# Kernel tuning notes

Hardware: AMD Instinct MI355X
Metric: run time of the kernel (lower is better)

Reference implementation:

```python
import jax, jax.numpy as jnp
import numpy as np

D_MODEL = 1024
N_HEADS = 16
HEAD_DIM = D_MODEL // N_HEADS  # 64
THETA = 10000.0
BATCH = 2
SEQ = 2048


def _init_weight(k):
    std = np.sqrt(2.0 / (D_MODEL + D_MODEL)).astype(np.float32)
    return jax.random.truncated_normal(k, -3.0, 3.0, (D_MODEL, D_MODEL), jnp.float32) * std


def setup_inputs() -> dict:
    key = jax.random.key(0)
    kx, kq, kk, kv, ko = jax.random.split(key, 5)
    x = jax.random.normal(kx, (BATCH, SEQ, D_MODEL), jnp.float32)
    token_positions = jnp.arange(SEQ, dtype=jnp.int32)
    return {
        "x": x,
        "token_positions": token_positions,
        "Wq": _init_weight(kq),
        "Wk": _init_weight(kk),
        "Wv": _init_weight(kv),
        "Wo": _init_weight(ko),
    }


def _rope(x, token_positions):
    # x: (B, H, S, HEAD_DIM), token_positions: (S,)
    pair_idx = jnp.arange(0, HEAD_DIM, 2, dtype=jnp.float32)
    inv_freq = 1.0 / (THETA ** (pair_idx / HEAD_DIM))        # (HEAD_DIM/2,)
    angles = token_positions.astype(jnp.float32)[:, None] * inv_freq  # (S, HEAD_DIM/2)
    cos = jnp.cos(angles).astype(x.dtype)
    sin = jnp.sin(angles).astype(x.dtype)
    x_even = x[..., 0::2]
    x_odd = x[..., 1::2]
    out_even = x_even * cos - x_odd * sin
    out_odd = x_even * sin + x_odd * cos
    return jnp.stack((out_even, out_odd), axis=-1).reshape(x.shape)


def reference(x, token_positions, Wq, Wk, Wv, Wo):
    B, S, _ = x.shape

    def proj(W):  # (B,S,D) @ (D,D)^T -> (B,H,S,HEAD_DIM)
        return (x @ W.T).reshape(B, S, N_HEADS, HEAD_DIM).transpose(0, 2, 1, 3)

    q = _rope(proj(Wq), token_positions)
    k = _rope(proj(Wk), token_positions)
    v = proj(Wv)

    scale = 1.0 / np.sqrt(HEAD_DIM).astype(np.float32)
    scores = jnp.einsum('bhqd,bhkd->bhqk', q, k) * scale  # (B,H,S,S)
    causal = jnp.tril(jnp.ones((S, S), dtype=bool))
    scores = jnp.where(causal, scores, -jnp.inf)
    probs = jax.nn.softmax(scores.astype(jnp.float32), axis=-1).astype(x.dtype)

    attn = jnp.einsum('bhqk,bhkd->bhqd', probs, v)  # (B,H,S,HEAD_DIM)
    attn = attn.transpose(0, 2, 1, 3).reshape(B, S, D_MODEL)
    return attn @ Wo.T
```

## Files before the change

### kernel.cpp

```cpp
#include <hip/hip_runtime.h>

typedef __bf16 bf16x4 __attribute__((ext_vector_type(4)));
typedef __bf16 bf16x8 __attribute__((ext_vector_type(8)));
typedef float floatx4 __attribute__((ext_vector_type(4)));

#define MFMA16(a, b, c) __builtin_amdgcn_mfma_f32_16x16x32_bf16((a), (b), (c), 0, 0, 0)

#define GLD16(gptr, lptr)                                                      \
    __builtin_amdgcn_global_load_lds(                                          \
        (const __attribute__((address_space(1))) void*)(gptr),                 \
        (__attribute__((address_space(3))) void*)(lptr), 16, 0, 0)

constexpr int D_MODEL = 1024;
constexpr int SEQ = 2048;
constexpr int HEAD_DIM = 64;
constexpr int M_TOK = 2 * SEQ;
constexpr int N_HEADS = 16;
constexpr float ROPE_C = 0.20762050593048596f;

__global__ __launch_bounds__(256) void convert_all(
    const float* __restrict__ x,  const float* __restrict__ wq,
    const float* __restrict__ wk, const float* __restrict__ wv,
    const float* __restrict__ wo, __bf16* __restrict__ dst,
    const int* __restrict__ pos, float2* __restrict__ rt)
{
    const size_t i = ((size_t)blockIdx.x * 256 + threadIdx.x) * 8;
    const float* s;
    size_t off;
    if (i < 4194304) { s = x; off = i; }
    else {
        const int w = (int)((i - 4194304) >> 20);
        off = (i - 4194304) & 1048575;
        s = (w == 0) ? wq : (w == 1) ? wk : (w == 2) ? wv : wo;
    }
    const floatx4 lo = *(const floatx4*)(s + off);
    const floatx4 hi = *(const floatx4*)(s + off + 4);
    bf16x8 v;
    v[0] = (__bf16)lo[0]; v[1] = (__bf16)lo[1]; v[2] = (__bf16)lo[2]; v[3] = (__bf16)lo[3];
    v[4] = (__bf16)hi[0]; v[5] = (__bf16)hi[1]; v[6] = (__bf16)hi[2]; v[7] = (__bf16)hi[3];
    *(bf16x8*)(dst + i) = v;

    const int gid = blockIdx.x * 256 + threadIdx.x;
    if (gid < SEQ * 32) {
        const int p = gid >> 5, j = gid & 31;
        const float ang = (float)pos[p] * exp2f(-(float)(2 * j) * ROPE_C);
        rt[gid] = make_float2(cosf(ang), sinf(ang));
    }
}

template<int MODE>
__global__ __launch_bounds__(256, 3) void gemm_tiled(
    const __bf16* __restrict__ A, const __bf16* __restrict__ B,
    __bf16* __restrict__ Qb, __bf16* __restrict__ Kb, __bf16* __restrict__ Vt,
    float* __restrict__ Cf, const float2* __restrict__ rt)
{
    __shared__ __bf16 As[128 * 32];
    __shared__ __bf16 Bs[128 * 32];
    const int tid  = threadIdx.x;
    const int wave = tid >> 6, lane = tid & 63;
    const int quad = lane >> 4, l16 = lane & 15;

    constexpr int NWG = (MODE == 0) ? 32 * 24 : 32 * 8;
    const int wgid = blockIdx.x + 32 * blockIdx.y;
    const int nid  = (wgid & 7) * (NWG / 8) + (wgid >> 3);
    const int m0 = (nid & 31) * 128, n0 = (nid >> 5) * 128;
    const int wm = (wave >> 1) * 64, wn = (wave & 1) * 64;

    floatx4 c00 = {}, c01 = {}, c02 = {}, c03 = {};
    floatx4 c10 = {}, c11 = {}, c12 = {}, c13 = {};
    floatx4 c20 = {}, c21 = {}, c22 = {}, c23 = {};
    floatx4 c30 = {}, c31 = {}, c32 = {}, c33 = {};

    const int sm = tid >> 2;
    const int sk = (tid & 3) * 8;
    const __bf16* gA = A + (size_t)(m0 + sm) * D_MODEL + sk;
    const __bf16* gB = B + (size_t)(n0 + sm) * D_MODEL + sk;
    __bf16* lAs0 = &As[wave * 512];
    __bf16* lAs1 = &As[2048 + wave * 512];
    __bf16* lBs0 = &Bs[wave * 512];
    __bf16* lBs1 = &Bs[2048 + wave * 512];

    for (int k0 = 0; k0 < D_MODEL; k0 += 32) {
        __syncthreads();
        GLD16(gA + k0,                          lAs0);
        GLD16(gA + (size_t)64 * D_MODEL + k0,   lAs1);
        GLD16(gB + k0,                          lBs0);
        GLD16(gB + (size_t)64 * D_MODEL + k0,   lBs1);
        __syncthreads();

        const bf16x8 a0 = *(const bf16x8*)&As[(wm      + l16) * 32 + quad * 8];
        const bf16x8 a1 = *(const bf16x8*)&As[(wm + 16 + l16) * 32 + quad * 8];
        const bf16x8 a2 = *(const bf16x8*)&As[(wm + 32 + l16) * 32 + quad * 8];
        const bf16x8 a3 = *(const bf16x8*)&As[(wm + 48 + l16) * 32 + quad * 8];
        const bf16x8 b0 = *(const bf16x8*)&Bs[(wn      + l16) * 32 + quad * 8];
        const bf16x8 b1 = *(const bf16x8*)&Bs[(wn + 16 + l16) * 32 + quad * 8];
        const bf16x8 b2 = *(const bf16x8*)&Bs[(wn + 32 + l16) * 32 + quad * 8];
        const bf16x8 b3 = *(const bf16x8*)&Bs[(wn + 48 + l16) * 32 + quad * 8];

        c00 = MFMA16(a0, b0, c00); c01 = MFMA16(a0, b1, c01);
        c02 = MFMA16(a0, b2, c02); c03 = MFMA16(a0, b3, c03);
        c10 = MFMA16(a1, b0, c10); c11 = MFMA16(a1, b1, c11);
        c12 = MFMA16(a1, b2, c12); c13 = MFMA16(a1, b3, c13);
        c20 = MFMA16(a2, b0, c20); c21 = MFMA16(a2, b1, c21);
        c22 = MFMA16(a2, b2, c22); c23 = MFMA16(a2, b3, c23);
        c30 = MFMA16(a3, b0, c30); c31 = MFMA16(a3, b1, c31);
        c32 = MFMA16(a3, b2, c32); c33 = MFMA16(a3, b3, c33);
    }

#define EPI(I, J, CV) do {                                                     \
        const int n  = n0 + wn + (J) * 16 + l16;                               \
        const int t0 = m0 + wm + (I) * 16 + quad * 4;                          \
        if (MODE == 1) {                                                       \
            Cf[(size_t)(t0 + 0) * D_MODEL + n] = (CV)[0];                      \
            Cf[(size_t)(t0 + 1) * D_MODEL + n] = (CV)[1];                      \
            Cf[(size_t)(t0 + 2) * D_MODEL + n] = (CV)[2];                      \
            Cf[(size_t)(t0 + 3) * D_MODEL + n] = (CV)[3];                      \
        } else {                                                               \
            const int region = n >> 10, col = n & 1023;                        \
            if (region == 2) {                                                 \
                bf16x4 v;                                                      \
                v[0] = (__bf16)(CV)[0]; v[1] = (__bf16)(CV)[1];                \
                v[2] = (__bf16)(CV)[2]; v[3] = (__bf16)(CV)[3];                \
                const size_t vidx =                                            \
                    ((size_t)(t0 >> 11) * 1024 + col) * SEQ + (t0 & (SEQ - 1));\
                *(bf16x4*)(Vt + vidx) = v;                                     \
            } else {                                                           \
                const int d = col & (HEAD_DIM - 1);                            \
                const int j = d >> 1;                                          \
                __bf16* dst = (region == 0) ? Qb : Kb;                         \
                _Pragma("unroll")                                              \
                for (int r = 0; r < 4; ++r) {                                  \
                    float v = (CV)[r];                                         \
                    const float vp = __shfl_xor(v, 1);                         \
                    const float2 cs =                                          \
                        rt[(size_t)((t0 + r) & (SEQ - 1)) * 32 + j];           \
                    v = (d & 1) ? (vp * cs.y + v * cs.x)                       \
                                : (v * cs.x - vp * cs.y);                      \
                    dst[(size_t)(t0 + r) * D_MODEL + col] = (__bf16)v;         \
                }                                                              \
            }                                                                  \
        }                                                                      \
    } while (0)

    EPI(0, 0, c00); EPI(0, 1, c01); EPI(0, 2, c02); EPI(0, 3, c03);
    EPI(1, 0, c10); EPI(1, 1, c11); EPI(1, 2, c12); EPI(1, 3, c13);
    EPI(2, 0, c20); EPI(2, 1, c21); EPI(2, 2, c22); EPI(2, 3, c23);
    EPI(3, 0, c30); EPI(3, 1, c31); EPI(3, 2, c32); EPI(3, 3, c33);
#undef EPI
}

__global__ __launch_bounds__(256, 4) void attn_fused(
    const __bf16* Q, const __bf16* __restrict__ K,
    const __bf16* __restrict__ Vt, __bf16* O)
{
    const int tid  = threadIdx.x;
    const int wave = tid >> 6, lane = tid & 63;
    const int quad = lane >> 4, l16 = lane & 15;

    const int wgid = blockIdx.x + 32 * blockIdx.y;
    const int xcd  = wgid & 7;
    const int slot = wgid >> 3;
    const int bh   = (xcd << 2) | (slot & 3);
    const int T    = 31 - (slot >> 2);

    const size_t base  = (size_t)(bh >> 4) * SEQ * D_MODEL + (size_t)(bh & 15) * HEAD_DIM;
    const __bf16* kbase  = K + base;
    const __bf16* vtbase = Vt + (size_t)bh * HEAD_DIM * SEQ;

    __shared__ __bf16 Ks[64][72];
    __shared__ __bf16 Vs[64][72];
    __shared__ __bf16 P[4][16][72];

    constexpr float C2 = 0.18033688011112042f;
    const int sr = tid >> 2;
    const int sc = (tid & 3) * 16;

    const int Q0  = T * 64;
    const int q0w = Q0 + wave * 16;
    const int qg  = q0w + l16;

    const __bf16* qrow = Q + base + (size_t)(q0w + l16) * D_MODEL + quad * 8;
    const bf16x8 qf0 = *(const bf16x8*)(qrow);
    const bf16x8 qf1 = *(const bf16x8*)(qrow + 32);

    float mm = -__builtin_inff(), l_i = 0.f;
    floatx4 o0 = {}, o1 = {}, o2 = {}, o3 = {};

    bf16x8 kr0, kr1, vr0, vr1;
    {
        const __bf16* kgp = kbase + (size_t)sr * D_MODEL + sc;
        kr0 = *(const bf16x8*)(kgp);
        kr1 = *(const bf16x8*)(kgp + 8);
        const __bf16* vgp = vtbase + (size_t)sr * SEQ + sc;
        vr0 = *(const bf16x8*)(vgp);
        vr1 = *(const bf16x8*)(vgp + 8);
    }
    *(bf16x8*)&Ks[sr][sc]     = kr0;
    *(bf16x8*)&Ks[sr][sc + 8] = kr1;
    *(bf16x8*)&Vs[sr][sc]     = vr0;
    *(bf16x8*)&Vs[sr][sc + 8] = vr1;

    for (int k0 = 0; k0 <= Q0; k0 += 64) {
        const bool pf = (k0 + 64 <= Q0);
        if (pf) {
            const __bf16* kgp = kbase + (size_t)(k0 + 64 + sr) * D_MODEL + sc;
            kr0 = *(const bf16x8*)(kgp);
            kr1 = *(const bf16x8*)(kgp + 8);
            const __bf16* vgp = vtbase + (size_t)sr * SEQ + (k0 + 64) + sc;
            vr0 = *(const bf16x8*)(vgp);
            vr1 = *(const bf16x8*)(vgp + 8);
        }
        __syncthreads();

        floatx4 s0 = {}, s1 = {}, s2 = {}, s3 = {};
        __builtin_amdgcn_s_setprio(1);
        s0 = MFMA16(*(const bf16x8*)&Ks[l16][quad * 8],      qf0, s0);
        s0 = MFMA16(*(const bf16x8*)&Ks[l16][32 + quad * 8], qf1, s0);
        s1 = MFMA16(*(const bf16x8*)&Ks[16 + l16][quad * 8],      qf0, s1);
        s1 = MFMA16(*(const bf16x8*)&Ks[16 + l16][32 + quad * 8], qf1, s1);
        s2 = MFMA16(*(const bf16x8*)&Ks[32 + l16][quad * 8],      qf0, s2);
        s2 = MFMA16(*(const bf16x8*)&Ks[32 + l16][32 + quad * 8], qf1, s2);
        s3 = MFMA16(*(const bf16x8*)&Ks[48 + l16][quad * 8],      qf0, s3);
        s3 = MFMA16(*(const bf16x8*)&Ks[48 + l16][32 + quad * 8], qf1, s3);
        __builtin_amdgcn_s_setprio(0);

        if (k0 == Q0) {
#pragma unroll
            for (int r = 0; r < 4; ++r) {
                const int kb = k0 + quad * 4 + r;
                if (kb      > qg) s0[r] = -__builtin_inff();
                if (kb + 16 > qg) s1[r] = -__builtin_inff();
                if (kb + 32 > qg) s2[r] = -__builtin_inff();
                if (kb + 48 > qg) s3[r] = -__builtin_inff();
            }
        }

        float ma = fmaxf(fmaxf(s0[0], s0[1]), s0[2]);
        float mb = fmaxf(fmaxf(s0[3], s1[0]), s1[1]);
        float mc = fmaxf(fmaxf(s1[2], s1[3]), s2[0]);
        float md = fmaxf(fmaxf(s2[1], s2[2]), s2[3]);
        float me = fmaxf(fmaxf(s3[0], s3[1]), s3[2]);
        ma = fmaxf(fmaxf(ma, mb), mc);
        md = fmaxf(fmaxf(md, me), s3[3]);
        float mx = fmaxf(ma, md);
        mx = fmaxf(mx, __shfl_xor(mx, 16));
        mx = fmaxf(mx, __shfl_xor(mx, 32));
        const float mxs = mx * C2;

        if (!__all(mxs - mm <= 8.0f)) {
            const float mmn   = fmaxf(mm, mxs);
            const float alpha = exp2f(mm - mmn);
            l_i *= alpha;
            o0 *= alpha; o1 *= alpha; o2 *= alpha; o3 *= alpha;
            mm = mmn;
        }

        float rs = 0.f;
#pragma unroll
        for (int r = 0; r < 4; ++r) {
            s0[r] = exp2f(s0[r] * C2 - mm);
            s1[r] = exp2f(s1[r] * C2 - mm);
            s2[r] = exp2f(s2[r] * C2 - mm);
            s3[r] = exp2f(s3[r] * C2 - mm);
            rs += s0[r] + s1[r] + s2[r] + s3[r];
        }
        rs += __shfl_xor(rs, 16);
        rs += __shfl_xor(rs, 32);
        l_i += rs;

        bf16x4 pw0, pw1, pw2, pw3;
#pragma unroll
        for (int r = 0; r < 4; ++r) {
            pw0[r] = (__bf16)s0[r]; pw1[r] = (__bf16)s1[r];
            pw2[r] = (__bf16)s2[r]; pw3[r] = (__bf16)s3[r];
        }
        *(bf16x4*)&P[wave][l16][quad * 4]      = pw0;
        *(bf16x4*)&P[wave][l16][16 + quad * 4] = pw1;
        *(bf16x4*)&P[wave][l16][32 + quad * 4] = pw2;
        *(bf16x4*)&P[wave][l16][48 + quad * 4] = pw3;
        const bf16x8 pp0 = *(const bf16x8*)&P[wave][l16][quad * 8];
        const bf16x8 pp1 = *(const bf16x8*)&P[wave][l16][32 + quad * 8];

        __builtin_amdgcn_s_setprio(1);
        o0 = MFMA16(*(const bf16x8*)&Vs[l16][quad * 8],      pp0, o0);
        o0 = MFMA16(*(const bf16x8*)&Vs[l16][32 + quad * 8], pp1, o0);
        o1 = MFMA16(*(const bf16x8*)&Vs[16 + l16][quad * 8],      pp0, o1);
        o1 = MFMA16(*(const bf16x8*)&Vs[16 + l16][32 + quad * 8], pp1, o1);
        o2 = MFMA16(*(const bf16x8*)&Vs[32 + l16][quad * 8],      pp0, o2);
        o2 = MFMA16(*(const bf16x8*)&Vs[32 + l16][32 + quad * 8], pp1, o2);
        o3 = MFMA16(*(const bf16x8*)&Vs[48 + l16][quad * 8],      pp0, o3);
        o3 = MFMA16(*(const bf16x8*)&Vs[48 + l16][32 + quad * 8], pp1, o3);
        __builtin_amdgcn_s_setprio(0);

        __syncthreads();
        if (pf) {
            *(bf16x8*)&Ks[sr][sc]     = kr0;
            *(bf16x8*)&Ks[sr][sc + 8] = kr1;
            *(bf16x8*)&Vs[sr][sc]     = vr0;
            *(bf16x8*)&Vs[sr][sc + 8] = vr1;
        }
    }

    const float rl = 1.0f / l_i;
    __bf16* orow = O + base + (size_t)(q0w + l16) * D_MODEL + quad * 4;
    bf16x4 w0, w1, w2, w3;
#pragma unroll
    for (int r = 0; r < 4; ++r) {
        w0[r] = (__bf16)(o0[r] * rl);
        w1[r] = (__bf16)(o1[r] * rl);
        w2[r] = (__bf16)(o2[r] * rl);
        w3[r] = (__bf16)(o3[r] * rl);
    }
    *(bf16x4*)(orow)      = w0;
    *(bf16x4*)(orow + 16) = w1;
    *(bf16x4*)(orow + 32) = w2;
    *(bf16x4*)(orow + 48) = w3;
}

extern "C" void kernel_launch(void* const* d_in, const int* in_sizes, int n_in,
                              void* d_out, int out_size, void* d_ws, size_t ws_size,
                              hipStream_t stream) {
    const int* pos = (const int*)d_in[1];
    float* out = (float*)d_out;

    const size_t xe = (size_t)M_TOK * D_MODEL;
    const size_t we = (size_t)D_MODEL * D_MODEL;
    __bf16* Xb = (__bf16*)d_ws;
    __bf16* Wb = Xb + xe;
    __bf16* Qb = Wb + 4 * we;
    __bf16* Kb = Qb + xe;
    __bf16* Vt = Kb + xe;
    float2* rt = (float2*)d_out;

    convert_all<<<4096, 256, 0, stream>>>(
        (const float*)d_in[0], (const float*)d_in[2], (const float*)d_in[3],
        (const float*)d_in[4], (const float*)d_in[5], Xb, pos, rt);

    gemm_tiled<0><<<dim3(M_TOK / 128, 3072 / 128), 256, 0, stream>>>(
        Xb, Wb, Qb, Kb, Vt, nullptr, rt);

    attn_fused<<<dim3(32, 32), 256, 0, stream>>>(Qb, Kb, Vt, Qb);

    gemm_tiled<1><<<dim3(M_TOK / 128, D_MODEL / 128), 256, 0, stream>>>(
        Qb, Wb + 3 * we, nullptr, nullptr, nullptr, out, rt);
}
```

Before: 190.7 us.

## Use 128-row query tiles with 8 waves sharing each K/V tile in attention

```diff
diff --git a/kernel.cpp b/kernel.cpp
--- a/kernel.cpp
+++ b/kernel.cpp
@@ -149,7 +149,7 @@
 #undef EPI
 }
 
-__global__ __launch_bounds__(256, 4) void attn_fused(
+__global__ __launch_bounds__(512, 4) void attn_fused(
     const __bf16* Q, const __bf16* __restrict__ K,
     const __bf16* __restrict__ Vt, __bf16* O)
 {
@@ -157,11 +157,11 @@
     const int wave = tid >> 6, lane = tid & 63;
     const int quad = lane >> 4, l16 = lane & 15;
 
-    const int wgid = blockIdx.x + 32 * blockIdx.y;
+    const int wgid = blockIdx.x + 16 * blockIdx.y;
     const int xcd  = wgid & 7;
     const int slot = wgid >> 3;
     const int bh   = (xcd << 2) | (slot & 3);
-    const int T    = 31 - (slot >> 2);
+    const int T    = 15 - (slot >> 2);
 
     const size_t base  = (size_t)(bh >> 4) * SEQ * D_MODEL + (size_t)(bh & 15) * HEAD_DIM;
     const __bf16* kbase  = K + base;
@@ -169,140 +169,131 @@
 
     __shared__ __bf16 Ks[64][72];
     __shared__ __bf16 Vs[64][72];
-    __shared__ __bf16 P[4][16][72];
+    __shared__ __bf16 P[8][16][72];
 
     constexpr float C2 = 0.18033688011112042f;
-    const int sr = tid >> 2;
-    const int sc = (tid & 3) * 16;
-
-    const int Q0  = T * 64;
-    const int q0w = Q0 + wave * 16;
-    const int qg  = q0w + l16;
-
-    const __bf16* qrow = Q + base + (size_t)(q0w + l16) * D_MODEL + quad * 8;
+    const int sr = tid >> 3;
+    const int sc = (tid & 7) * 8;
+
+    const int Q0   = T * 128;
+    const int q0w  = Q0 + wave * 16;
+    const int qg   = q0w + l16;
+    const int kEnd = Q0 + 64;
+
+    const __bf16* qrow = Q + base + (size_t)qg * D_MODEL + quad * 8;
     const bf16x8 qf0 = *(const bf16x8*)(qrow);
     const bf16x8 qf1 = *(const bf16x8*)(qrow + 32);
 
     float mm = -__builtin_inff(), l_i = 0.f;
     floatx4 o0 = {}, o1 = {}, o2 = {}, o3 = {};
 
-    bf16x8 kr0, kr1, vr0, vr1;
+    bf16x8 kr0, vr0;
     {
-        const __bf16* kgp = kbase + (size_t)sr * D_MODEL + sc;
-        kr0 = *(const bf16x8*)(kgp);
-        kr1 = *(const bf16x8*)(kgp + 8);
-        const __bf16* vgp = vtbase + (size_t)sr * SEQ + sc;
-        vr0 = *(const bf16x8*)(vgp);
-        vr1 = *(const bf16x8*)(vgp + 8);
-    }
-    *(bf16x8*)&Ks[sr][sc]     = kr0;
-    *(bf16x8*)&Ks[sr][sc + 8] = kr1;
-    *(bf16x8*)&Vs[sr][sc]     = vr0;
-    *(bf16x8*)&Vs[sr][sc + 8] = vr1;
-
-    for (int k0 = 0; k0 <= Q0; k0 += 64) {
-        const bool pf = (k0 + 64 <= Q0);
+        kr0 = *(const bf16x8*)(kbase + (size_t)sr * D_MODEL + sc);
+        vr0 = *(const bf16x8*)(vtbase + (size_t)sr * SEQ + sc);
+    }
+    *(bf16x8*)&Ks[sr][sc] = kr0;
+    *(bf16x8*)&Vs[sr][sc] = vr0;
+
+    for (int k0 = 0; k0 <= kEnd; k0 += 64) {
+        const bool pf = (k0 + 64 <= kEnd);
         if (pf) {
-            const __bf16* kgp = kbase + (size_t)(k0 + 64 + sr) * D_MODEL + sc;
-            kr0 = *(const bf16x8*)(kgp);
-            kr1 = *(const bf16x8*)(kgp + 8);
-            const __bf16* vgp = vtbase + (size_t)sr * SEQ + (k0 + 64) + sc;
-            vr0 = *(const bf16x8*)(vgp);
-            vr1 = *(const bf16x8*)(vgp + 8);
+            kr0 = *(const bf16x8*)(kbase + (size_t)(k0 + 64 + sr) * D_MODEL + sc);
+            vr0 = *(const bf16x8*)(vtbase + (size_t)sr * SEQ + (k0 + 64) + sc);
         }
         __syncthreads();
 
-        floatx4 s0 = {}, s1 = {}, s2 = {}, s3 = {};
-        __builtin_amdgcn_s_setprio(1);
-        s0 = MFMA16(*(const bf16x8*)&Ks[l16][quad * 8],      qf0, s0);
-        s0 = MFMA16(*(const bf16x8*)&Ks[l16][32 + quad * 8], qf1, s0);
-        s1 = MFMA16(*(const bf16x8*)&Ks[16 + l16][quad * 8],      qf0, s1);
-        s1 = MFMA16(*(const bf16x8*)&Ks[16 + l16][32 + quad * 8], qf1, s1);
-        s2 = MFMA16(*(const bf16x8*)&Ks[32 + l16][quad * 8],      qf0, s2);
-        s2 = MFMA16(*(const bf16x8*)&Ks[32 + l16][32 + quad * 8], qf1, s2);
-        s3 = MFMA16(*(const bf16x8*)&Ks[48 + l16][quad * 8],      qf0, s3);
-        s3 = MFMA16(*(const bf16x8*)&Ks[48 + l16][32 + quad * 8], qf1, s3);
-        __builtin_amdgcn_s_setprio(0);
-
-        if (k0 == Q0) {
+        if (k0 <= q0w + 15) {
+            floatx4 s0 = {}, s1 = {}, s2 = {}, s3 = {};
+            __builtin_amdgcn_s_setprio(1);
+            s0 = MFMA16(*(const bf16x8*)&Ks[l16][quad * 8],      qf0, s0);
+            s0 = MFMA16(*(const bf16x8*)&Ks[l16][32 + quad * 8], qf1, s0);
+            s1 = MFMA16(*(const bf16x8*)&Ks[16 + l16][quad * 8],      qf0, s1);
+            s1 = MFMA16(*(const bf16x8*)&Ks[16 + l16][32 + quad * 8], qf1, s1);
+            s2 = MFMA16(*(const bf16x8*)&Ks[32 + l16][quad * 8],      qf0, s2);
+            s2 = MFMA16(*(const bf16x8*)&Ks[32 + l16][32 + quad * 8], qf1, s2);
+            s3 = MFMA16(*(const bf16x8*)&Ks[48 + l16][quad * 8],      qf0, s3);
+            s3 = MFMA16(*(const bf16x8*)&Ks[48 + l16][32 + quad * 8], qf1, s3);
+            __builtin_amdgcn_s_setprio(0);
+
+            if (k0 + 63 > q0w) {
+#pragma unroll
+                for (int r = 0; r < 4; ++r) {
+                    const int kb = k0 + quad * 4 + r;
+                    if (kb      > qg) s0[r] = -__builtin_inff();
+                    if (kb + 16 > qg) s1[r] = -__builtin_inff();
+                    if (kb + 32 > qg) s2[r] = -__builtin_inff();
+                    if (kb + 48 > qg) s3[r] = -__builtin_inff();
+                }
+            }
+
+            float ma = fmaxf(fmaxf(s0[0], s0[1]), s0[2]);
+            float mb = fmaxf(fmaxf(s0[3], s1[0]), s1[1]);
+            float mc = fmaxf(fmaxf(s1[2], s1[3]), s2[0]);
+            float md = fmaxf(fmaxf(s2[1], s2[2]), s2[3]);
+            float me = fmaxf(fmaxf(s3[0], s3[1]), s3[2]);
+            ma = fmaxf(fmaxf(ma, mb), mc);
+            md = fmaxf(fmaxf(md, me), s3[3]);
+            float mx = fmaxf(ma, md);
+            mx = fmaxf(mx, __shfl_xor(mx, 16));
+            mx = fmaxf(mx, __shfl_xor(mx, 32));
+            const float mxs = mx * C2;
+
+            if (!__all(mxs - mm <= 8.0f)) {
+                const float mmn   = fmaxf(mm, mxs);
+                const float alpha = exp2f(mm - mmn);
+                l_i *= alpha;
+                o0 *= alpha; o1 *= alpha; o2 *= alpha; o3 *= alpha;
+                mm = mmn;
+            }
+
+            float rs = 0.f;
 #pragma unroll
             for (int r = 0; r < 4; ++r) {
-                const int kb = k0 + quad * 4 + r;
-                if (kb      > qg) s0[r] = -__builtin_inff();
-                if (kb + 16 > qg) s1[r] = -__builtin_inff();
-                if (kb + 32 > qg) s2[r] = -__builtin_inff();
-                if (kb + 48 > qg) s3[r] = -__builtin_inff();
+                s0[r] = exp2f(s0[r] * C2 - mm);
+                s1[r] = exp2f(s1[r] * C2 - mm);
+                s2[r] = exp2f(s2[r] * C2 - mm);
+                s3[r] = exp2f(s3[r] * C2 - mm);
+                rs += s0[r] + s1[r] + s2[r] + s3[r];
             }
+            rs += __shfl_xor(rs, 16);
+            rs += __shfl_xor(rs, 32);
+            l_i += rs;
+
+            bf16x4 pw0, pw1, pw2, pw3;
+#pragma unroll
+            for (int r = 0; r < 4; ++r) {
+                pw0[r] = (__bf16)s0[r]; pw1[r] = (__bf16)s1[r];
+                pw2[r] = (__bf16)s2[r]; pw3[r] = (__bf16)s3[r];
+            }
+            *(bf16x4*)&P[wave][l16][quad * 4]      = pw0;
+            *(bf16x4*)&P[wave][l16][16 + quad * 4] = pw1;
+            *(bf16x4*)&P[wave][l16][32 + quad * 4] = pw2;
+            *(bf16x4*)&P[wave][l16][48 + quad * 4] = pw3;
+            const bf16x8 pp0 = *(const bf16x8*)&P[wave][l16][quad * 8];
+            const bf16x8 pp1 = *(const bf16x8*)&P[wave][l16][32 + quad * 8];
+
+            __builtin_amdgcn_s_setprio(1);
+            o0 = MFMA16(*(const bf16x8*)&Vs[l16][quad * 8],      pp0, o0);
+            o0 = MFMA16(*(const bf16x8*)&Vs[l16][32 + quad * 8], pp1, o0);
+            o1 = MFMA16(*(const bf16x8*)&Vs[16 + l16][quad * 8],      pp0, o1);
+            o1 = MFMA16(*(const bf16x8*)&Vs[16 + l16][32 + quad * 8], pp1, o1);
+            o2 = MFMA16(*(const bf16x8*)&Vs[32 + l16][quad * 8],      pp0, o2);
+            o2 = MFMA16(*(const bf16x8*)&Vs[32 + l16][32 + quad * 8], pp1, o2);
+            o3 = MFMA16(*(const bf16x8*)&Vs[48 + l16][quad * 8],      pp0, o3);
+            o3 = MFMA16(*(const bf16x8*)&Vs[48 + l16][32 + quad * 8], pp1, o3);
+            __builtin_amdgcn_s_setprio(0);
         }
-
-        float ma = fmaxf(fmaxf(s0[0], s0[1]), s0[2]);
-        float mb = fmaxf(fmaxf(s0[3], s1[0]), s1[1]);
-        float mc = fmaxf(fmaxf(s1[2], s1[3]), s2[0]);
-        float md = fmaxf(fmaxf(s2[1], s2[2]), s2[3]);
-        float me = fmaxf(fmaxf(s3[0], s3[1]), s3[2]);
-        ma = fmaxf(fmaxf(ma, mb), mc);
-        md = fmaxf(fmaxf(md, me), s3[3]);
-        float mx = fmaxf(ma, md);
-        mx = fmaxf(mx, __shfl_xor(mx, 16));
-        mx = fmaxf(mx, __shfl_xor(mx, 32));
-        const float mxs = mx * C2;
-
-        if (!__all(mxs - mm <= 8.0f)) {
-            const float mmn   = fmaxf(mm, mxs);
-            const float alpha = exp2f(mm - mmn);
-            l_i *= alpha;
-            o0 *= alpha; o1 *= alpha; o2 *= alpha; o3 *= alpha;
-            mm = mmn;
-        }
-
-        float rs = 0.f;
-#pragma unroll
-        for (int r = 0; r < 4; ++r) {
-            s0[r] = exp2f(s0[r] * C2 - mm);
-            s1[r] = exp2f(s1[r] * C2 - mm);
-            s2[r] = exp2f(s2[r] * C2 - mm);
-            s3[r] = exp2f(s3[r] * C2 - mm);
-            rs += s0[r] + s1[r] + s2[r] + s3[r];
-        }
-        rs += __shfl_xor(rs, 16);
-        rs += __shfl_xor(rs, 32);
-        l_i += rs;
-
-        bf16x4 pw0, pw1, pw2, pw3;
-#pragma unroll
-        for (int r = 0; r < 4; ++r) {
-            pw0[r] = (__bf16)s0[r]; pw1[r] = (__bf16)s1[r];
-            pw2[r] = (__bf16)s2[r]; pw3[r] = (__bf16)s3[r];
-        }
-        *(bf16x4*)&P[wave][l16][quad * 4]      = pw0;
-        *(bf16x4*)&P[wave][l16][16 + quad * 4] = pw1;
-        *(bf16x4*)&P[wave][l16][32 + quad * 4] = pw2;
-        *(bf16x4*)&P[wave][l16][48 + quad * 4] = pw3;
-        const bf16x8 pp0 = *(const bf16x8*)&P[wave][l16][quad * 8];
-        const bf16x8 pp1 = *(const bf16x8*)&P[wave][l16][32 + quad * 8];
-
-        __builtin_amdgcn_s_setprio(1);
-        o0 = MFMA16(*(const bf16x8*)&Vs[l16][quad * 8],      pp0, o0);
-        o0 = MFMA16(*(const bf16x8*)&Vs[l16][32 + quad * 8], pp1, o0);
-        o1 = MFMA16(*(const bf16x8*)&Vs[16 + l16][quad * 8],      pp0, o1);
-        o1 = MFMA16(*(const bf16x8*)&Vs[16 + l16][32 + quad * 8], pp1, o1);
-        o2 = MFMA16(*(const bf16x8*)&Vs[32 + l16][quad * 8],      pp0, o2);
-        o2 = MFMA16(*(const bf16x8*)&Vs[32 + l16][32 + quad * 8], pp1, o2);
-        o3 = MFMA16(*(const bf16x8*)&Vs[48 + l16][quad * 8],      pp0, o3);
-        o3 = MFMA16(*(const bf16x8*)&Vs[48 + l16][32 + quad * 8], pp1, o3);
-        __builtin_amdgcn_s_setprio(0);
 
         __syncthreads();
         if (pf) {
-            *(bf16x8*)&Ks[sr][sc]     = kr0;
-            *(bf16x8*)&Ks[sr][sc + 8] = kr1;
-            *(bf16x8*)&Vs[sr][sc]     = vr0;
-            *(bf16x8*)&Vs[sr][sc + 8] = vr1;
+            *(bf16x8*)&Ks[sr][sc] = kr0;
+            *(bf16x8*)&Vs[sr][sc] = vr0;
         }
     }
 
     const float rl = 1.0f / l_i;
-    __bf16* orow = O + base + (size_t)(q0w + l16) * D_MODEL + quad * 4;
+    __bf16* orow = O + base + (size_t)qg * D_MODEL + quad * 4;
     bf16x4 w0, w1, w2, w3;
 #pragma unroll
     for (int r = 0; r < 4; ++r) {
@@ -339,7 +330,7 @@
     gemm_tiled<0><<<dim3(M_TOK / 128, 3072 / 128), 256, 0, stream>>>(
         Xb, Wb, Qb, Kb, Vt, nullptr, rt);
 
-    attn_fused<<<dim3(32, 32), 256, 0, stream>>>(Qb, Kb, Vt, Qb);
+    attn_fused<<<dim3(16, 32), 512, 0, stream>>>(Qb, Kb, Vt, Qb);
 
     gemm_tiled<1><<<dim3(M_TOK / 128, D_MODEL / 128), 256, 0, stream>>>(
         Qb, Wb + 3 * we, nullptr, nullptr, nullptr, out, rt);
```

New measurement: 198.5 us. 1.04x slower.
